# Optimization experiments

Hardware: AMD Instinct MI355X
Metric: run time of the kernel (lower is better)

## Reference

```python
import jax, jax.numpy as jnp
import numpy as np

ALPHA = 0.1
BETA = 1.1
NUM_CLASSES = 16
EPS = 1e-8  # matches torch cosine_similarity eps
BATCH = 131072
DIM = 512


def setup_inputs() -> dict:
    key = jax.random.key(0)
    k1, k2 = jax.random.split(key)
    embeddings = jax.random.normal(k1, (BATCH, DIM), dtype=jnp.float32)
    labels = jax.random.randint(k2, (BATCH,), 0, NUM_CLASSES)
    return {"embeddings": embeddings, "labels": labels}


def _cos_dist(a, b):
    # a: [M, D], b: [N, D] -> 1 - cosine_similarity, shape [M, N]
    an = a / jnp.maximum(jnp.linalg.norm(a, axis=-1, keepdims=True), EPS)
    bn = b / jnp.maximum(jnp.linalg.norm(b, axis=-1, keepdims=True), EPS)
    return 1.0 - an @ bn.T


def reference(embeddings, labels):
    C = NUM_CLASSES
    N = embeddings.shape[0]
    dt = embeddings.dtype

    # class centroids (dummy anchors) via scatter-mean
    cnt = jax.ops.segment_sum(jnp.ones((N,), dt), labels, num_segments=C)  # [C]
    sums = jax.ops.segment_sum(embeddings, labels, num_segments=C)        # [C, D]
    centroids = sums / jnp.maximum(cnt, 1.0)[:, None]
    present = cnt > 0

    # close class pairs: i < j, both present, centroid distance <= beta
    pd = _cos_dist(centroids, centroids)                    # [C, C]
    upper = jnp.triu(jnp.ones((C, C), bool), k=1)
    pairmask = upper & (pd <= BETA) & present[:, None] & present[None, :]
    pm = pairmask.astype(dt)
    deg = pm.sum(1) + pm.sum(0)                             # pairs involving each class

    # distances from every centroid to every sample
    D = _cos_dist(centroids, embeddings)                    # [C, N]

    # intra: each sample of class c contributes relu(d(cent_c, x) - alpha),
    # once per close pair involving c
    d_own = D[labels, jnp.arange(N)]                        # [N]
    intra_sum = jnp.sum(deg[labels] * jax.nn.relu(d_own - ALPHA))

    # inter: S[c, c'] = sum over samples with label c' of relu(beta - d(cent_c, x))
    S = jax.ops.segment_sum(jax.nn.relu(BETA - D).T, labels, num_segments=C).T  # [C, C]
    inter_sum = jnp.sum(pm * (S + S.T))

    # number of terms in each loss list: sum over pairs of (cnt_i + cnt_j)
    count = jnp.sum(deg * cnt)
    denom = jnp.maximum(count, 1.0)
    num_pairs = pm.sum()

    loss = jnp.where(num_pairs > 0, intra_sum / denom + inter_sum / denom, 0.0)
    return loss
```

## Files before the change

### kernel.cpp

```cpp
#include <hip/hip_runtime.h>

constexpr float kAlpha = 0.1f;
constexpr float kBeta  = 1.1f;
constexpr int   kC     = 16;
constexpr int   kD     = 512;
constexpr float kEps   = 1e-8f;

constexpr int SUMS_OFF = 0;
constexpr int CNT_OFF  = 8192;
constexpr int TOT_OFF  = 8208;
constexpr int CN_OFF   = 8224;
constexpr int MSK_OFF  = 16416;
constexpr int SCL_OFF  = 16432;
constexpr int ZERO_FLOATS = 8209;

__device__ __forceinline__ float dot4(float4 a, float4 b) {
    return a.x * b.x + a.y * b.y + a.z * b.z + a.w * b.w;
}

__global__ __launch_bounds__(512) void k1_sums(const float* __restrict__ emb,
                                               const int* __restrict__ labels,
                                               float* __restrict__ sums,
                                               float* __restrict__ cnt,
                                               int N, int rpb) {
    __shared__ float lacc[kC * kD];
    __shared__ float lcnt[kC];
    int tid = threadIdx.x;
    int wave = tid >> 6, lane = tid & 63;
    int half = wave & 1;

    for (int i = tid; i < kC * kD; i += 512) lacc[i] = 0.f;
    if (tid < kC) lcnt[tid] = 0.f;
    __syncthreads();

    float4 acc[kC];
#pragma unroll
    for (int c = 0; c < kC; ++c) acc[c] = make_float4(0.f, 0.f, 0.f, 0.f);
    float cacc = 0.f;

    const float4* e4 = (const float4*)emb;
    long long h0 = 2LL * blockIdx.x * rpb;
    long long hEnd = min(h0 + 2LL * rpb, 2LL * (long long)N);

    for (long long h = h0 + wave; h < hEnd; h += 16) {
        long long hb = h + 8;
        bool vb = (hb < hEnd);
        int rowA = (int)(h >> 1);
        int rowB = vb ? (int)(hb >> 1) : rowA;
        int lA = labels[rowA];
        int lB = labels[rowB];
        float4 vA = e4[(size_t)rowA * 128 + half * 64 + lane];
        float4 vB = e4[(size_t)rowB * 128 + half * 64 + lane];
        if (!vb) vB = make_float4(0.f, 0.f, 0.f, 0.f);
#pragma unroll
        for (int c = 0; c < kC; ++c) {
            if (lA == c) { acc[c].x += vA.x; acc[c].y += vA.y; acc[c].z += vA.z; acc[c].w += vA.w; }
            if (lB == c) { acc[c].x += vB.x; acc[c].y += vB.y; acc[c].z += vB.z; acc[c].w += vB.w; }
        }
        if (half == 0 && lane < kC) {
            cacc += (lA == lane ? 1.f : 0.f) + ((vb && lB == lane) ? 1.f : 0.f);
        }
    }

#pragma unroll
    for (int c = 0; c < kC; ++c) {
        float* p = &lacc[c * kD + half * 256 + lane * 4];
        atomicAdd(p + 0, acc[c].x);
        atomicAdd(p + 1, acc[c].y);
        atomicAdd(p + 2, acc[c].z);
        atomicAdd(p + 3, acc[c].w);
    }
    if (half == 0 && lane < kC) atomicAdd(&lcnt[lane], cacc);
    __syncthreads();
    for (int i = tid; i < kC * kD; i += 512) atomicAdd(&sums[i], lacc[i]);
    if (tid < kC) atomicAdd(&cnt[tid], lcnt[tid]);
}

__global__ __launch_bounds__(256) void k2_cent(const float* __restrict__ sums,
                                               const float* __restrict__ cnt_g,
                                               float* __restrict__ cn_g,
                                               unsigned* __restrict__ mask_g,
                                               float* __restrict__ scal) {
    __shared__ __align__(16) float lcn[kC * kD];
    __shared__ float lcnt[kC];
    __shared__ float red[256];
    __shared__ float norms[kC];
    __shared__ float pdm[kC * kC];
    int tid = threadIdx.x;
    if (tid < kC) lcnt[tid] = cnt_g[tid];
    __syncthreads();

    int c = tid >> 4, sub = tid & 15;
    float invc = 1.f / fmaxf(lcnt[c], 1.f);
    float sq = 0.f;
    for (int d = sub; d < kD; d += 16) {
        float v = sums[c * kD + d] * invc;
        lcn[c * kD + d] = v;
        sq += v * v;
    }
    red[tid] = sq;
    __syncthreads();
    if (tid < kC) {
        float t = 0.f;
        for (int k = 0; k < 16; ++k) t += red[tid * 16 + k];
        norms[tid] = fmaxf(sqrtf(t), kEps);
    }
    __syncthreads();
    for (int i = tid; i < kC * kD; i += 256) {
        float v = lcn[i] / norms[i / kD];
        lcn[i] = v;
        cn_g[i] = v;
    }
    __syncthreads();
    int pi = tid >> 4, pj = tid & 15;
    float dot = 0.f;
    for (int dd = 0; dd < kD; ++dd) {
        int d = (dd + tid) & (kD - 1);
        dot += lcn[pi * kD + d] * lcn[pj * kD + d];
    }
    pdm[tid] = 1.f - dot;
    __syncthreads();
    if (tid == 0) {
        unsigned m[kC];
        for (int a = 0; a < kC; ++a) m[a] = 0u;
        float npairs = 0.f;
        for (int a = 0; a < kC; ++a)
            for (int b = a + 1; b < kC; ++b) {
                bool close = (pdm[a * kC + b] <= kBeta) && (lcnt[a] > 0.f) && (lcnt[b] > 0.f);
                if (close) { m[a] |= 1u << b; m[b] |= 1u << a; npairs += 1.f; }
            }
        float count = 0.f;
        for (int a = 0; a < kC; ++a) {
            mask_g[a] = m[a];
            count += (float)__popc(m[a]) * lcnt[a];
        }
        scal[0] = fmaxf(count, 1.f);
        scal[1] = npairs;
    }
}

constexpr int TR = 32;
__global__ __launch_bounds__(512, 2) void k3_main(const float* __restrict__ emb,
                                                  const int* __restrict__ labels,
                                                  const float* __restrict__ cn_g,
                                                  const unsigned* __restrict__ mask_g,
                                                  float* __restrict__ total,
                                                  int N, int rpb) {
    __shared__ __align__(16) float4 xbuf[TR * 128];
    __shared__ unsigned lmask[kC];
    __shared__ float wsum[8];
    int tid = threadIdx.x;
    int wave = tid >> 6, lane = tid & 63;
    int g = lane >> 4, j = lane & 15;

    const float4* w4 = (const float4*)cn_g;
    float4 wreg[4][8];
#pragma unroll
    for (int c = 0; c < 4; ++c)
#pragma unroll
        for (int i = 0; i < 8; ++i)
            wreg[c][i] = w4[(4 * g + c) * 128 + i * 16 + j];
    if (tid < kC) lmask[tid] = mask_g[tid];

    int r0 = blockIdx.x * rpb;
    int r1 = min(r0 + rpb, N);
    float priv = 0.f;

    const float4* src = (const float4*)emb;
    float4 st[8];

    if (r0 < r1) {
        int avail = (r1 - r0) * 128;
#pragma unroll
        for (int k = 0; k < 8; ++k) {
            int idx = k * 512 + tid;
            st[k] = (idx < avail) ? src[(size_t)r0 * 128 + idx] : make_float4(0.f, 0.f, 0.f, 0.f);
        }
#pragma unroll
        for (int k = 0; k < 8; ++k) xbuf[k * 512 + tid] = st[k];
    }
    __syncthreads();

    for (int rt = r0; rt < r1; rt += TR) {
        int ntile = rt + TR;
        bool more = (ntile < r1);
        if (more) {
            int avail = (r1 - ntile) * 128;
#pragma unroll
            for (int k = 0; k < 8; ++k) {
                int idx = k * 512 + tid;
                st[k] = (idx < avail) ? src[(size_t)ntile * 128 + idx] : make_float4(0.f, 0.f, 0.f, 0.f);
            }
        }

        int rows = min(TR, r1 - rt);
        for (int rr = wave; rr < rows; rr += 8) {
            int row = rt + rr;
            int lab = labels[row];
            const float4* xr = &xbuf[rr * 128];
            float d0 = 0.f, d1 = 0.f, d2 = 0.f, d3 = 0.f, nrm = 0.f;
#pragma unroll
            for (int i = 0; i < 8; ++i) {
                float4 x = xr[i * 16 + j];
                nrm += dot4(x, x);
                d0 += dot4(x, wreg[0][i]);
                d1 += dot4(x, wreg[1][i]);
                d2 += dot4(x, wreg[2][i]);
                d3 += dot4(x, wreg[3][i]);
            }
#pragma unroll
            for (int m = 1; m < 16; m <<= 1) {
                d0 += __shfl_xor(d0, m, 64);
                d1 += __shfl_xor(d1, m, 64);
                d2 += __shfl_xor(d2, m, 64);
                d3 += __shfl_xor(d3, m, 64);
                nrm += __shfl_xor(nrm, m, 64);
            }
            if (j == 0) {
                unsigned mm = lmask[lab];
                float inv = 1.f / fmaxf(sqrtf(nrm), kEps);
                float s = 0.f;
                float dv[4] = {d0, d1, d2, d3};
#pragma unroll
                for (int c = 0; c < 4; ++c) {
                    int cg = 4 * g + c;
                    float dd = 1.f - dv[c] * inv;
                    if ((mm >> cg) & 1u) s += fmaxf(kBeta - dd, 0.f);
                    if (cg == lab) s += (float)__popc(mm) * fmaxf(dd - kAlpha, 0.f);
                }
                priv += s;
            }
        }
        __syncthreads();
        if (more) {
#pragma unroll
            for (int k = 0; k < 8; ++k) xbuf[k * 512 + tid] = st[k];
        }
        __syncthreads();
    }

#pragma unroll
    for (int off = 32; off > 0; off >>= 1) priv += __shfl_down(priv, off, 64);
    if (lane == 0) wsum[wave] = priv;
    __syncthreads();
    if (tid == 0) {
        float t = 0.f;
#pragma unroll
        for (int w = 0; w < 8; ++w) t += wsum[w];
        atomicAdd(total, t);
    }
}

__global__ void k4_final(const float* __restrict__ total,
                         const float* __restrict__ scal,
                         float* __restrict__ out) {
    out[0] = (scal[1] > 0.f) ? (total[0] / scal[0]) : 0.f;
}

extern "C" void kernel_launch(void* const* d_in, const int* in_sizes, int n_in,
                              void* d_out, int out_size, void* d_ws, size_t ws_size,
                              hipStream_t stream) {
    const float* emb = (const float*)d_in[0];
    const int* labels = (const int*)d_in[1];
    int N = in_sizes[0] / kD;

    float* ws = (float*)d_ws;
    float* sums = ws + SUMS_OFF;
    float* cnt = ws + CNT_OFF;
    float* total = ws + TOT_OFF;
    float* cn = ws + CN_OFF;
    unsigned* mask = (unsigned*)(ws + MSK_OFF);
    float* scal = ws + SCL_OFF;

    hipMemsetAsync(d_ws, 0, ZERO_FLOATS * sizeof(float), stream);

    int blocks1 = 512;
    int rpb1 = (N + blocks1 - 1) / blocks1;
    k1_sums<<<blocks1, 512, 0, stream>>>(emb, labels, sums, cnt, N, rpb1);

    k2_cent<<<1, 256, 0, stream>>>(sums, cnt, cn, mask, scal);

    int blocks3 = 256;
    int rpb3 = (N + blocks3 - 1) / blocks3;
    k3_main<<<blocks3, 512, 0, stream>>>(emb, labels, cn, mask, total, N, rpb3);

    k4_final<<<1, 1, 0, stream>>>(total, scal, (float*)d_out);
}
```

Baseline: 557.2 us.

## Restructure class-sum kernel: wave-per-row with uniform label switch and prefetch

The centroid-sum kernel now assigns one whole 512-float row per wave, with each lane holding two float4 slices and separate accumulator sets. A wave-uniform label read through readfirstlane drives a switch, so only one accumulator is updated per row instead of 16 predicated compares. The next row is software-prefetched into registers while the current one is accumulated. Block size drops to 256 threads, which doubles per-thread accumulator registers and may lower occupancy and memory-level parallelism.

```diff
diff --git a/kernel.cpp b/kernel.cpp
--- a/kernel.cpp
+++ b/kernel.cpp
@@ -17,8 +17,11 @@
 __device__ __forceinline__ float dot4(float4 a, float4 b) {
     return a.x * b.x + a.y * b.y + a.z * b.z + a.w * b.w;
 }
-
-__global__ __launch_bounds__(512) void k1_sums(const float* __restrict__ emb,
+__device__ __forceinline__ void add4(float4& a, float4 b) {
+    a.x += b.x; a.y += b.y; a.z += b.z; a.w += b.w;
+}
+
+__global__ __launch_bounds__(256) void k1_sums(const float* __restrict__ emb,
                                                const int* __restrict__ labels,
                                                float* __restrict__ sums,
                                                float* __restrict__ cnt,
@@ -27,52 +30,77 @@
     __shared__ float lcnt[kC];
     int tid = threadIdx.x;
     int wave = tid >> 6, lane = tid & 63;
-    int half = wave & 1;
-
-    for (int i = tid; i < kC * kD; i += 512) lacc[i] = 0.f;
+
+    for (int i = tid; i < kC * kD; i += 256) lacc[i] = 0.f;
     if (tid < kC) lcnt[tid] = 0.f;
-    __syncthreads();
-
-    float4 acc[kC];
-#pragma unroll
-    for (int c = 0; c < kC; ++c) acc[c] = make_float4(0.f, 0.f, 0.f, 0.f);
+
+    float4 accA[kC], accB[kC];
+#pragma unroll
+    for (int c = 0; c < kC; ++c) {
+        accA[c] = make_float4(0.f, 0.f, 0.f, 0.f);
+        accB[c] = make_float4(0.f, 0.f, 0.f, 0.f);
+    }
     float cacc = 0.f;
 
     const float4* e4 = (const float4*)emb;
-    long long h0 = 2LL * blockIdx.x * rpb;
-    long long hEnd = min(h0 + 2LL * rpb, 2LL * (long long)N);
-
-    for (long long h = h0 + wave; h < hEnd; h += 16) {
-        long long hb = h + 8;
-        bool vb = (hb < hEnd);
-        int rowA = (int)(h >> 1);
-        int rowB = vb ? (int)(hb >> 1) : rowA;
-        int lA = labels[rowA];
-        int lB = labels[rowB];
-        float4 vA = e4[(size_t)rowA * 128 + half * 64 + lane];
-        float4 vB = e4[(size_t)rowB * 128 + half * 64 + lane];
-        if (!vb) vB = make_float4(0.f, 0.f, 0.f, 0.f);
-#pragma unroll
-        for (int c = 0; c < kC; ++c) {
-            if (lA == c) { acc[c].x += vA.x; acc[c].y += vA.y; acc[c].z += vA.z; acc[c].w += vA.w; }
-            if (lB == c) { acc[c].x += vB.x; acc[c].y += vB.y; acc[c].z += vB.z; acc[c].w += vB.w; }
-        }
-        if (half == 0 && lane < kC) {
-            cacc += (lA == lane ? 1.f : 0.f) + ((vb && lB == lane) ? 1.f : 0.f);
-        }
-    }
-
+    int r0 = blockIdx.x * rpb;
+    int r1 = min(r0 + rpb, N);
+
+#define ACC1(c) { add4(accA[c], a0); add4(accB[c], a1); }
+#define DO_SWITCH(l)                                                        \
+    switch (l) {                                                            \
+        case 0:  ACC1(0);  break; case 1:  ACC1(1);  break;                 \
+        case 2:  ACC1(2);  break; case 3:  ACC1(3);  break;                 \
+        case 4:  ACC1(4);  break; case 5:  ACC1(5);  break;                 \
+        case 6:  ACC1(6);  break; case 7:  ACC1(7);  break;                 \
+        case 8:  ACC1(8);  break; case 9:  ACC1(9);  break;                 \
+        case 10: ACC1(10); break; case 11: ACC1(11); break;                 \
+        case 12: ACC1(12); break; case 13: ACC1(13); break;                 \
+        case 14: ACC1(14); break; default: ACC1(15); break;                 \
+    }
+
+    int r = r0 + wave;
+    bool v = (r < r1);
+    int rc = v ? r : 0;
+    float4 a0 = e4[(size_t)rc * 128 + lane];
+    float4 a1 = e4[(size_t)rc * 128 + 64 + lane];
+    int la = labels[rc];
+
+    while (v) {
+        int rn = r + 4;
+        bool vn = (rn < r1);
+        int rcn = vn ? rn : 0;
+        float4 b0 = e4[(size_t)rcn * 128 + lane];
+        float4 b1 = e4[(size_t)rcn * 128 + 64 + lane];
+        int lb = labels[rcn];
+
+        int l = __builtin_amdgcn_readfirstlane(la);
+        DO_SWITCH(l);
+        cacc += (lane < kC && l == lane) ? 1.f : 0.f;
+
+        a0 = b0; a1 = b1; la = lb;
+        r = rn; v = vn;
+    }
+#undef DO_SWITCH
+#undef ACC1
+
+    __syncthreads();
 #pragma unroll
     for (int c = 0; c < kC; ++c) {
-        float* p = &lacc[c * kD + half * 256 + lane * 4];
-        atomicAdd(p + 0, acc[c].x);
-        atomicAdd(p + 1, acc[c].y);
-        atomicAdd(p + 2, acc[c].z);
-        atomicAdd(p + 3, acc[c].w);
-    }
-    if (half == 0 && lane < kC) atomicAdd(&lcnt[lane], cacc);
-    __syncthreads();
-    for (int i = tid; i < kC * kD; i += 512) atomicAdd(&sums[i], lacc[i]);
+        float* pA = &lacc[c * kD + 4 * lane];
+        atomicAdd(pA + 0, accA[c].x);
+        atomicAdd(pA + 1, accA[c].y);
+        atomicAdd(pA + 2, accA[c].z);
+        atomicAdd(pA + 3, accA[c].w);
+        float* pB = &lacc[c * kD + 256 + 4 * lane];
+        atomicAdd(pB + 0, accB[c].x);
+        atomicAdd(pB + 1, accB[c].y);
+        atomicAdd(pB + 2, accB[c].z);
+        atomicAdd(pB + 3, accB[c].w);
+    }
+    if (lane < kC) atomicAdd(&lcnt[lane], cacc);
+    __syncthreads();
+    for (int i = tid; i < kC * kD; i += 256) atomicAdd(&sums[i], lacc[i]);
     if (tid < kC) atomicAdd(&cnt[tid], lcnt[tid]);
 }
 
@@ -276,7 +304,7 @@
 
     int blocks1 = 512;
     int rpb1 = (N + blocks1 - 1) / blocks1;
-    k1_sums<<<blocks1, 512, 0, stream>>>(emb, labels, sums, cnt, N, rpb1);
+    k1_sums<<<blocks1, 256, 0, stream>>>(emb, labels, sums, cnt, N, rpb1);
 
     k2_cent<<<1, 256, 0, stream>>>(sums, cnt, cn, mask, scal);
 
```

Result: slower. 580.1 us (+4.1%).
